# Optimization experiments

Measured on AMD Instinct MI355X. Metric: run time of the kernel, lower is better.

Reference implementation:

```python
import jax, jax.numpy as jnp
import numpy as np

EMBED = 768; HEADS = 12; DH = 64; DEPTH = 6; MLP = 3072
PATCH = (4, 16, 16)
N_PATCH = 2048          # (32/4)*(256/16)*(256/16)
N_REAL = N_PATCH + 1    # + cls token
S_PAD = 4096            # padded to multiple of max segment length
SEGS = [128, 256, 512, 1024, 2048]
RATIOS = [1, 2, 4, 8, 16]
NEG = -1e9


def _ln(x, w, b, eps=1e-5):
    m = jnp.mean(x, -1, keepdims=True)
    v = jnp.mean((x - m) ** 2, -1, keepdims=True)
    return (x - m) / jnp.sqrt(v + eps) * w + b


def dilated_attn(x, wq, bq, wk, bk, wv, bv, wo, bo):
    """LongNet dilated attention: per (segment w, ratio r) branch, split the
    sequence into segments of length w, keep every r-th token with a per-head
    offset (h % r), run dense attention inside the sparse segment, then combine
    branches per position/head with softmax-denominator (lse) weights."""
    B, S, E = x.shape
    q = (x @ wq + bq).reshape(B, S, HEADS, DH)
    k = (x @ wk + bk).reshape(B, S, HEADS, DH)
    v = (x @ wv + bv).reshape(B, S, HEADS, DH)
    scale = 1.0 / np.sqrt(DH).astype(np.float32)
    harr = jnp.arange(HEADS)[:, None]
    outs, lses = [], []
    for w, r in zip(SEGS, RATIOS):
        ns, m = S // w, w // r
        idx = (jnp.arange(HEADS)[:, None] % r) + r * jnp.arange(m)[None, :]  # [H, m]

        def seg(t):
            t = t.reshape(B, ns, w, HEADS, DH).transpose(0, 1, 3, 2, 4)  # B,ns,H,w,D
            return jnp.take_along_axis(t, idx[None, None, :, :, None], axis=3)

        qs, ks, vs = seg(q), seg(k), seg(v)  # [B, ns, H, m, D]
        pos = (jnp.arange(ns) * w)[:, None, None] + idx[None]  # [ns, H, m]
        kmask = jnp.where(pos < N_REAL, 0.0, NEG)  # mask padded keys
        sc = jnp.einsum('bnhqd,bnhkd->bnhqk', qs, ks) * scale + kmask[None, :, :, None, :]
        lse = jax.nn.logsumexp(sc, axis=-1)  # [B, ns, H, m]
        o = jnp.einsum('bnhqk,bnhkd->bnhqd', jax.nn.softmax(sc, axis=-1), vs)
        of = jnp.zeros((B, ns, HEADS, w, DH), x.dtype).at[:, :, harr, idx, :].set(o)
        lf = jnp.full((B, ns, HEADS, w), NEG, x.dtype).at[:, :, harr, idx].set(lse)
        outs.append(of.transpose(0, 1, 3, 2, 4).reshape(B, S, HEADS, DH))
        lses.append(lf.transpose(0, 1, 3, 2).reshape(B, S, HEADS))
    O = jnp.stack(outs)   # [Br, B, S, H, D]
    L = jnp.stack(lses)   # [Br, B, S, H]
    wts = jnp.exp(L - jnp.max(L, 0))
    wts = wts / jnp.sum(wts, 0)
    out = jnp.sum(O * wts[..., None], 0).reshape(B, S, E)
    return out @ wo + bo


def setup_inputs() -> dict:
    key = jax.random.key(0)
    ks = jax.random.split(key, 16)
    f = lambda k, shape: (0.02 * jax.random.normal(k, shape)).astype(jnp.float32)
    z = lambda *s: jnp.zeros(s, jnp.float32)
    o = lambda *s: jnp.ones(s, jnp.float32)
    return {
        'x': jax.random.normal(ks[0], (1, 1, 32, 256, 256), dtype=jnp.float32),
        'conv_w': f(ks[1], (EMBED, 1) + PATCH),
        'conv_b': z(EMBED),
        'cls_token': f(ks[2], (1, 1, EMBED)),
        'pos_embed': f(ks[3], (1, N_REAL, EMBED)),
        'ln1_w': o(DEPTH, EMBED), 'ln1_b': z(DEPTH, EMBED),
        'wq': f(ks[4], (DEPTH, EMBED, EMBED)), 'bq': z(DEPTH, EMBED),
        'wk': f(ks[5], (DEPTH, EMBED, EMBED)), 'bk': z(DEPTH, EMBED),
        'wv': f(ks[6], (DEPTH, EMBED, EMBED)), 'bv': z(DEPTH, EMBED),
        'wo': f(ks[7], (DEPTH, EMBED, EMBED)), 'bo': z(DEPTH, EMBED),
        'ln2_w': o(DEPTH, EMBED), 'ln2_b': z(DEPTH, EMBED),
        'w1': f(ks[8], (DEPTH, EMBED, MLP)), 'b1': z(DEPTH, MLP),
        'w2': f(ks[9], (DEPTH, MLP, EMBED)), 'b2': z(DEPTH, EMBED),
        'lnf_w': o(EMBED), 'lnf_b': z(EMBED),
    }


def reference(x, conv_w, conv_b, cls_token, pos_embed, ln1_w, ln1_b,
              wq, bq, wk, bk, wv, bv, wo, bo, ln2_w, ln2_b,
              w1, b1, w2, b2, lnf_w, lnf_b):
    # 3D patch embed: Conv3d stride=kernel=patch, then flatten spatial -> tokens
    p = jax.lax.conv_general_dilated(
        x, conv_w, window_strides=PATCH, padding='VALID',
        dimension_numbers=('NCDHW', 'OIDHW', 'NCDHW'))
    p = p + conv_b[None, :, None, None, None]
    B = p.shape[0]
    tok = p.reshape(B, EMBED, -1).transpose(0, 2, 1)  # [B, N_PATCH, E]
    tok = tok + pos_embed[:, 1:, :]
    cls = cls_token + pos_embed[:, :1, :]
    h = jnp.concatenate([jnp.broadcast_to(cls, (B, 1, EMBED)), tok], axis=1)
    h = jnp.pad(h, ((0, 0), (0, S_PAD - N_REAL), (0, 0)))  # pad to segment multiple

    params = {'ln1_w': ln1_w, 'ln1_b': ln1_b, 'wq': wq, 'bq': bq, 'wk': wk,
              'bk': bk, 'wv': wv, 'bv': bv, 'wo': wo, 'bo': bo,
              'ln2_w': ln2_w, 'ln2_b': ln2_b, 'w1': w1, 'b1': b1,
              'w2': w2, 'b2': b2}

    def layer(h, pr):
        a = dilated_attn(_ln(h, pr['ln1_w'], pr['ln1_b']),
                         pr['wq'], pr['bq'], pr['wk'], pr['bk'],
                         pr['wv'], pr['bv'], pr['wo'], pr['bo'])
        h = h + a
        f = _ln(h, pr['ln2_w'], pr['ln2_b'])
        f = jax.nn.gelu(f @ pr['w1'] + pr['b1'], approximate=False) @ pr['w2'] + pr['b2']
        return h + f, None

    h, _ = jax.lax.scan(layer, h, params)
    return _ln(h[:, 0], lnf_w, lnf_b)  # [B, EMBED]
```

## Files before the change

kernel.cpp:

```cpp
#include <hip/hip_runtime.h>
#include <math.h>

#define EMBED 768
#define HEADS 12
#define DH 64
#define DEPTH 6
#define MLP_DIM 3072
#define N_REAL 2049
#define SP 2112
#define SPAD 2176
#define NEGV (-1e9f)

typedef __attribute__((ext_vector_type(8))) short short8;
typedef __attribute__((ext_vector_type(4))) float f32x4;
typedef float lds_row_t[33];

__device__ __forceinline__ unsigned short f2bf(float f) {
    union { float f; unsigned u; } x; x.f = f;
    unsigned r = x.u + 0x7FFF + ((x.u >> 16) & 1);
    return (unsigned short)(r >> 16);
}
__device__ __forceinline__ float bf2f(unsigned short s) {
    union { unsigned u; float f; } x; x.u = (unsigned)s << 16;
    return x.f;
}

__device__ __forceinline__ float fast_gelu(float v) {
    const float ax = fabsf(v) * 0.70710678118654752f;
    const float tt = 1.0f / (1.0f + 0.3275911f * ax);
    const float poly = tt * (0.254829592f + tt * (-0.284496736f + tt * (1.421413741f
                       + tt * (-1.453152027f + tt * 1.061405429f))));
    float er = 1.0f - poly * __expf(-ax * ax);
    er = (v < 0.0f) ? -er : er;
    return 0.5f * v * (1.0f + er);
}

__device__ __forceinline__ size_t pidx(int mj, int k, int nkt) {
    return (((size_t)(mj >> 4) * nkt + (k >> 5)) << 9) + (size_t)((((k >> 3) & 3) * 16 + (mj & 15)) * 8 + (k & 7));
}

__device__ __forceinline__ void im2col_body(const float* __restrict__ x,
                                            unsigned short* __restrict__ p, int pi) {
    const int d = pi >> 8, rr = (pi >> 4) & 15, cc = pi & 15;
    const int t = threadIdx.x;
    #pragma unroll
    for (int u = 0; u < 4; ++u) {
        int i = u * 256 + t;
        int kd = i >> 8, kr = (i >> 4) & 15, kc = i & 15;
        float v = x[(size_t)(d * 4 + kd) * 65536 + (rr * 16 + kr) * 256 + (cc * 16 + kc)];
        p[pidx(pi, i, 32)] = f2bf(v);
    }
}

__global__ void im2col_kernel(const float* __restrict__ x, unsigned short* __restrict__ p) {
    im2col_body(x, p, blockIdx.x);
}

__device__ __forceinline__ void pack_KN_body(lds_row_t* lf, const float* __restrict__ src,
                                             unsigned short* __restrict__ dst,
                                             int N, int K, int bn, int bk) {
    const int t = threadIdx.x;
    {
        const int kk = t >> 3, ch = t & 7;
        const float4* s = (const float4*)(src + (size_t)(bk * 32 + kk) * N + bn * 128 + ch * 16);
        float4 v0 = s[0], v1 = s[1], v2 = s[2], v3 = s[3];
        float tmp[16];
        ((float4*)tmp)[0] = v0; ((float4*)tmp)[1] = v1; ((float4*)tmp)[2] = v2; ((float4*)tmp)[3] = v3;
        const int cidx = (kk + 4 * ch) & 31;
        #pragma unroll
        for (int u = 0; u < 16; ++u) lf[ch * 16 + u][cidx] = tmp[u];
    }
    __syncthreads();
    const int nkt = K >> 5;
    const int cg = t >> 5;
    const int lbase = t & 31;
    const int rot = 4 * cg;
    unsigned short* o = dst + (((size_t)(bn * 8 + cg) * nkt + bk) << 9);
    #pragma unroll
    for (int q = 0; q < 2; ++q) {
        const int l = lbase + 32 * q;
        const int col = cg * 16 + (l & 15), kb = (l >> 4) * 8;
        unsigned short ov[8];
        #pragma unroll
        for (int e = 0; e < 8; ++e) ov[e] = f2bf(lf[col][(kb + e + rot) & 31]);
        *(short8*)(o + l * 8) = *(short8*)ov;
    }
    __syncthreads();
}

__device__ __forceinline__ void pack_piece(lds_row_t* lf, int r,
                                           const float* wq, const float* wk,
                                           const float* wv, const float* wo,
                                           const float* w1s, const float* w2s,
                                           unsigned short* qkv_pk, unsigned short* o_pk,
                                           unsigned short* w1_pk, unsigned short* w2_pk) {
    if (r < 576) {
        const int m = r / 144, rr = r % 144;
        const float* src = (m == 0) ? wq : (m == 1) ? wk : (m == 2) ? wv : wo;
        unsigned short* dst = (m < 3) ? qkv_pk + (size_t)m * EMBED * EMBED : o_pk;
        pack_KN_body(lf, src, dst, EMBED, EMBED, rr % 6, rr / 6);
    } else if (r < 1152) {
        const int rr = r - 576;
        pack_KN_body(lf, w1s, w1_pk, MLP_DIM, EMBED, rr % 24, rr / 24);
    } else {
        const int rr = r - 1152;
        pack_KN_body(lf, w2s, w2_pk, EMBED, MLP_DIM, rr % 6, rr / 6);
    }
}

__global__ void pack_all_kernel(const float* __restrict__ wq, const float* __restrict__ wk,
                                const float* __restrict__ wv, const float* __restrict__ wo,
                                const float* __restrict__ w1s, const float* __restrict__ w2s,
                                unsigned short* __restrict__ qkv_pk, unsigned short* __restrict__ o_pk,
                                unsigned short* __restrict__ w1_pk, unsigned short* __restrict__ w2_pk) {
    __shared__ float lf[128][33];
    pack_piece(lf, blockIdx.x, wq, wk, wv, wo, w1s, w2s, qkv_pk, o_pk, w1_pk, w2_pk);
}

__device__ __forceinline__ void pack_NK_body(lds_row_t* lf, const float* __restrict__ src,
                                             unsigned short* __restrict__ dst,
                                             int N, int K, int bn, int bk) {
    const int t = threadIdx.x;
    {
        const int row = t >> 1, hf = t & 1;
        const float4* s = (const float4*)(src + (size_t)(bn * 128 + row) * K + bk * 32 + hf * 16);
        float4 v0 = s[0], v1 = s[1], v2 = s[2], v3 = s[3];
        float tmp[16];
        ((float4*)tmp)[0] = v0; ((float4*)tmp)[1] = v1; ((float4*)tmp)[2] = v2; ((float4*)tmp)[3] = v3;
        #pragma unroll
        for (int u = 0; u < 16; ++u) lf[row][hf * 16 + u] = tmp[u];
    }
    __syncthreads();
    const int nkt = K >> 5;
    const int cg = t >> 5;
    const int lbase = t & 31;
    unsigned short* o = dst + (((size_t)(bn * 8 + cg) * nkt + bk) << 9);
    #pragma unroll
    for (int q = 0; q < 2; ++q) {
        const int l = lbase + 32 * q;
        const int col = cg * 16 + (l & 15), kb = (l >> 4) * 8;
        unsigned short ov[8];
        #pragma unroll
        for (int e = 0; e < 8; ++e) ov[e] = f2bf(lf[col][kb + e]);
        *(short8*)(o + l * 8) = *(short8*)ov;
    }
    __syncthreads();
}

__global__ void pack_NK_kernel(const float* __restrict__ src, unsigned short* __restrict__ dst,
                               int N, int K) {
    __shared__ float lf[128][33];
    pack_NK_body(lf, src, dst, N, K, blockIdx.x, blockIdx.y);
}

__device__ __forceinline__ void init_misc_body(int i,
                                 const float* __restrict__ bq, const float* __restrict__ bk,
                                 const float* __restrict__ bv, float* __restrict__ bqkv,
                                 const float* __restrict__ cls, const float* __restrict__ pos,
                                 float* __restrict__ h, float* __restrict__ tmp) {
    if (i < DEPTH * 2304) {
        int L = i / 2304, j = i - L * 2304;
        float v = (j < 768) ? bq[L * 768 + j] : (j < 1536) ? bk[L * 768 + j - 768] : bv[L * 768 + j - 1536];
        bqkv[i] = v;
    }
    int j = i - DEPTH * 2304;
    if (j >= 0 && j < EMBED) h[j] = cls[j] + pos[j];
    int k2 = j - EMBED;
    if (k2 >= 0 && k2 < 4 * EMBED)
        tmp[(size_t)(k2 / EMBED) * SP * EMBED + (k2 % EMBED)] = 0.0f;
}

__global__ void init_misc_kernel(const float* __restrict__ bq, const float* __restrict__ bk,
                                 const float* __restrict__ bv, float* __restrict__ bqkv,
                                 const float* __restrict__ cls, const float* __restrict__ pos,
                                 float* __restrict__ h, float* __restrict__ tmp) {
    init_misc_body(blockIdx.x * 256 + threadIdx.x, bq, bk, bv, bqkv, cls, pos, h, tmp);
}

__device__ __forceinline__ void pos_copy_body(const float* __restrict__ pos,
                                              float* __restrict__ h, int r) {
    const size_t base = (size_t)(r + 1) * EMBED;
    const int t = threadIdx.x;
    h[base + t]       = pos[base + t];
    h[base + t + 256] = pos[base + t + 256];
    h[base + t + 512] = pos[base + t + 512];
}

__global__ void pos_copy_kernel(const float* __restrict__ pos, float* __restrict__ h) {
    pos_copy_body(pos, h, blockIdx.x);
}

__global__ void prep_mega_kernel(const float* __restrict__ x, const float* __restrict__ conv_w,
                                 const float* __restrict__ wq, const float* __restrict__ wk,
                                 const float* __restrict__ wv, const float* __restrict__ wo,
                                 const float* __restrict__ w1s, const float* __restrict__ w2s,
                                 const float* __restrict__ bq, const float* __restrict__ bk,
                                 const float* __restrict__ bv, const float* __restrict__ cls,
                                 const float* __restrict__ pos,
                                 unsigned short* __restrict__ patch_pk,
                                 unsigned short* __restrict__ convw_pk,
                                 float* __restrict__ bqkv, float* __restrict__ h,
                                 float* __restrict__ tmp,
                                 unsigned short* __restrict__ qkv_pk, unsigned short* __restrict__ o_pk,
                                 unsigned short* __restrict__ w1_pk, unsigned short* __restrict__ w2_pk) {
    __shared__ float lf[128][33];
    const int fid = blockIdx.x;
    const size_t EE = (size_t)EMBED * EMBED, EM = (size_t)EMBED * MLP_DIM;
    if (fid < 6 * 1728) {
        const int lid = fid / 1728, r = fid % 1728;
        pack_piece(lf, r, wq + lid * EE, wk + lid * EE, wv + lid * EE, wo + lid * EE,
                   w1s + lid * EM, w2s + lid * EM,
                   qkv_pk + (size_t)lid * 3 * EE, o_pk + lid * EE,
                   w1_pk + lid * EM, w2_pk + lid * EM);
    } else if (fid < 6 * 1728 + 192) {
        const int r = fid - 6 * 1728;
        pack_NK_body(lf, conv_w, convw_pk, EMBED, 1024, r % 6, r / 6);
    } else if (fid < 6 * 1728 + 192 + 2048) {
        im2col_body(x, patch_pk, fid - (6 * 1728 + 192));
    } else if (fid < 6 * 1728 + 192 + 2048 + 69) {
        const int r = fid - (6 * 1728 + 192 + 2048);
        init_misc_body(r * 256 + threadIdx.x, bq, bk, bv, bqkv, cls, pos, h, tmp);
    } else {
        pos_copy_body(pos, h, fid - (6 * 1728 + 192 + 2048 + 69));
    }
}

template<bool PACKED>
__global__ void ln_res_kernel(float* __restrict__ h, const float* __restrict__ tmp, int nt,
                              void* __restrict__ outv,
                              const float* __restrict__ w, const float* __restrict__ b,
                              int M) {
    int row = blockIdx.x;
    if (row >= M) return;
    const size_t base = (size_t)row * EMBED;
    int tid = threadIdx.x;
    float v0 = h[base + tid], v1 = h[base + tid + 256], v2 = h[base + tid + 512];
    for (int c = 0; c < nt; ++c) {
        const float* tc = tmp + (size_t)c * SP * EMBED + base;
        v0 += tc[tid]; v1 += tc[tid + 256]; v2 += tc[tid + 512];
    }
    h[base + tid] = v0; h[base + tid + 256] = v1; h[base + tid + 512] = v2;
    __shared__ float red[4];
    float s = v0 + v1 + v2;
    #pragma unroll
    for (int o = 32; o > 0; o >>= 1) s += __shfl_down(s, o);
    if ((tid & 63) == 0) red[tid >> 6] = s;
    __syncthreads();
    float mean = (red[0] + red[1] + red[2] + red[3]) * (1.0f / 768.0f);
    __syncthreads();
    float d0 = v0 - mean, d1 = v1 - mean, d2 = v2 - mean;
    float q2 = d0 * d0 + d1 * d1 + d2 * d2;
    #pragma unroll
    for (int o = 32; o > 0; o >>= 1) q2 += __shfl_down(q2, o);
    if ((tid & 63) == 0) red[tid >> 6] = q2;
    __syncthreads();
    float var = (red[0] + red[1] + red[2] + red[3]) * (1.0f / 768.0f);
    float rstd = 1.0f / sqrtf(var + 1e-5f);
    float o0 = d0 * rstd * w[tid]       + b[tid];
    float o1 = d1 * rstd * w[tid + 256] + b[tid + 256];
    float o2 = d2 * rstd * w[tid + 512] + b[tid + 512];
    if (PACKED) {
        unsigned short* o = (unsigned short*)outv;
        o[pidx(row, tid,       24)] = f2bf(o0);
        o[pidx(row, tid + 256, 24)] = f2bf(o1);
        o[pidx(row, tid + 512, 24)] = f2bf(o2);
    } else {
        float* orow = (float*)outv + (size_t)row * EMBED;
        orow[tid] = o0; orow[tid + 256] = o1; orow[tid + 512] = o2;
    }
}

template<int ACT, int MODE>
__global__ __launch_bounds__(256)
void gemm_bf16(const unsigned short* __restrict__ Apk, const unsigned short* __restrict__ Bpk,
               const float* __restrict__ bias, void* __restrict__ Cv,
               int M, int N, int K, int nx, int ny, int nz) {
    const int nwg = nx * ny * nz;
    const int fid = blockIdx.x;
    const int xcd = fid & 7, slot = fid >> 3;
    const int qq = nwg >> 3, rr2 = nwg & 7;
    const int orig = (xcd < rr2 ? xcd * (qq + 1) : rr2 * (qq + 1) + (xcd - rr2) * qq) + slot;
    const int bx = orig % nx;
    const int tzy = orig / nx;
    const int bz = tzy % nz;
    const int by = tzy / nz;

    const int tid = threadIdx.x;
    const int lane = tid & 63;
    const int w4 = tid >> 6;
    const int wm = w4 >> 1, wn = w4 & 1;
    const int row0 = by * 128 + wm * 64, col0 = bx * 128 + wn * 64;
    const int nktT = K >> 5;
    const int nk = nktT / nz;
    const int t0 = bz * nk;

    f32x4 acc[4][4];
    #pragma unroll
    for (int mi = 0; mi < 4; ++mi)
        #pragma unroll
        for (int ni = 0; ni < 4; ++ni)
            #pragma unroll
            for (int j = 0; j < 4; ++j) acc[mi][ni][j] = 0.0f;

    const unsigned short* Ab[4];
    const unsigned short* Bb[4];
    #pragma unroll
    for (int i = 0; i < 4; ++i) {
        Ab[i] = Apk + (((size_t)(by * 8 + wm * 4 + i) * nktT + t0) << 9) + lane * 8;
        Bb[i] = Bpk + (((size_t)(bx * 8 + wn * 4 + i) * nktT + t0) << 9) + lane * 8;
    }

    auto LOADT = [&](int t, short8* aa, short8* bb) {
        #pragma unroll
        for (int i = 0; i < 4; ++i) {
            aa[i] = *(const short8*)(Ab[i] + (size_t)t * 512);
            bb[i] = *(const short8*)(Bb[i] + (size_t)t * 512);
        }
    };
    auto MF = [&](short8* aa, short8* bb) {
        #pragma unroll
        for (int mi = 0; mi < 4; ++mi)
            #pragma unroll
            for (int ni = 0; ni < 4; ++ni)
                acc[mi][ni] = __builtin_amdgcn_mfma_f32_16x16x32_bf16(aa[mi], bb[ni], acc[mi][ni], 0, 0, 0);
    };

    short8 A0[4], B0[4], A1[4], B1[4];
    LOADT(0, A0, B0);
    for (int t = 0; t < nk; t += 2) {
        LOADT(t + 1, A1, B1);
        MF(A0, B0);
        if (t + 2 < nk) LOADT(t + 2, A0, B0);
        MF(A1, B1);
    }

    float* Cf = (float*)Cv + (MODE == 0 ? (size_t)bz * SP * EMBED : 0);
    unsigned short* Cb = (unsigned short*)Cv;
    const int ln15 = lane & 15, kq = lane >> 4;
    const int nktN = N >> 5;
    const bool addb = (bz == 0);
    #pragma unroll
    for (int mi = 0; mi < 4; ++mi) {
        #pragma unroll
        for (int ni = 0; ni < 4; ++ni) {
            const int col = col0 + ni * 16 + ln15;
            const float bb = addb ? bias[col] : 0.0f;
            #pragma unroll
            for (int j = 0; j < 4; ++j) {
                const int row = row0 + mi * 16 + kq * 4 + j;
                if (row < M) {
                    float v = acc[mi][ni][j] + bb;
                    if (ACT == 1) v = fast_gelu(v);
                    if (MODE == 0)      Cf[(size_t)row * N + col] = v;
                    else if (MODE == 2) Cb[(size_t)row * N + col] = f2bf(v);
                    else                Cb[pidx(row, col, nktN)] = f2bf(v);
                }
            }
        }
    }
}

__global__ __launch_bounds__(256, 1)
void attn_kernel(const unsigned short* __restrict__ qkv,
                 unsigned short* __restrict__ Obr, float* __restrict__ Lbr) {
    const int bx = blockIdx.x, hh = blockIdx.y;
    int b, n;
    if      (bx < 17) { b = 0; n = bx; }
    else if (bx < 26) { b = 1; n = bx - 17; }
    else if (bx < 31) { b = 2; n = bx - 26; }
    else if (bx < 34) { b = 3; n = bx - 31; }
    else              { b = 4; n = bx - 34; }
    const int r = 1 << b;
    const int segw = 128 << b;
    const int base = n * segw + (hh & (r - 1));

    __shared__ __attribute__((aligned(16))) unsigned short VT[64 * 128];
    __shared__ __attribute__((aligned(16))) unsigned short Pl[128 * 128];

    const int tid = threadIdx.x;

    {
        const int key = tid >> 1, dh2 = (tid & 1) * 32;
        const int pos = base + r * key;
        const bool val = pos < N_REAL;
        const unsigned short* vsrc = qkv + (size_t)(val ? pos : 0) * 2304 + 1536 + hh * 64 + dh2;
        #pragma unroll
        for (int u = 0; u < 4; ++u) {
            short8 vv = ((const short8*)vsrc)[u];
            #pragma unroll
            for (int e = 0; e < 8; ++e) {
                const int d = dh2 + u * 8 + e;
                VT[(d * 256 + ((key * 2) ^ ((d & 7) << 4))) >> 1] =
                    val ? (unsigned short)vv[e] : (unsigned short)0;
            }
        }
    }
    __syncthreads();

    const int lane = tid & 63, wv = tid >> 6;
    const int ln15 = lane & 15, kq = lane >> 4;

    f32x4 sc[2][8];
    #pragma unroll
    for (int mi = 0; mi < 2; ++mi)
        #pragma unroll
        for (int ni = 0; ni < 8; ++ni)
            #pragma unroll
            for (int j = 0; j < 4; ++j) sc[mi][ni][j] = 0.0f;

    #pragma unroll
    for (int kt = 0; kt < 2; ++kt) {
        short8 qfr[2], kfr[8];
        #pragma unroll
        for (int mi = 0; mi < 2; ++mi) {
            const int pos = base + r * (wv * 32 + mi * 16 + ln15);
            qfr[mi] = *(const short8*)(qkv + (size_t)(pos < N_REAL ? pos : 0) * 2304
                                       + hh * 64 + kt * 32 + kq * 8);
        }
        #pragma unroll
        for (int ni = 0; ni < 8; ++ni) {
            const int pos = base + r * (ni * 16 + ln15);
            kfr[ni] = *(const short8*)(qkv + (size_t)(pos < N_REAL ? pos : 0) * 2304
                                       + 768 + hh * 64 + kt * 32 + kq * 8);
        }
        #pragma unroll
        for (int mi = 0; mi < 2; ++mi)
            #pragma unroll
            for (int ni = 0; ni < 8; ++ni)
                sc[mi][ni] = __builtin_amdgcn_mfma_f32_16x16x32_bf16(qfr[mi], kfr[ni], sc[mi][ni], 0, 0, 0);
    }

    #pragma unroll
    for (int ni = 0; ni < 8; ++ni) {
        const bool kval = (base + r * (ni * 16 + ln15)) < N_REAL;
        #pragma unroll
        for (int mi = 0; mi < 2; ++mi)
            #pragma unroll
            for (int j = 0; j < 4; ++j)
                sc[mi][ni][j] = kval ? sc[mi][ni][j] * 0.125f : NEGV;
    }

    float rsum[2][4];
    #pragma unroll
    for (int mi = 0; mi < 2; ++mi) {
        #pragma unroll
        for (int j = 0; j < 4; ++j) {
            float mx = sc[mi][0][j];
            #pragma unroll
            for (int ni = 1; ni < 8; ++ni) mx = fmaxf(mx, sc[mi][ni][j]);
            mx = fmaxf(mx, __shfl_xor(mx, 1));
            mx = fmaxf(mx, __shfl_xor(mx, 2));
            mx = fmaxf(mx, __shfl_xor(mx, 4));
            mx = fmaxf(mx, __shfl_xor(mx, 8));
            float sm = 0.f;
            #pragma unroll
            for (int ni = 0; ni < 8; ++ni) {
                float e = __expf(sc[mi][ni][j] - mx);
                sc[mi][ni][j] = e;
                sm += e;
            }
            sm += __shfl_xor(sm, 1);
            sm += __shfl_xor(sm, 2);
            sm += __shfl_xor(sm, 4);
            sm += __shfl_xor(sm, 8);
            rsum[mi][j] = sm;
            const int prow = wv * 32 + mi * 16 + kq * 4 + j;
            const int qpos = base + r * prow;
            if (ln15 == 0 && qpos < N_REAL)
                Lbr[((size_t)b * SP + qpos) * HEADS + hh] = mx + logf(sm);
        }
    }

    #pragma unroll
    for (int mi = 0; mi < 2; ++mi)
        #pragma unroll
        for (int j = 0; j < 4; ++j) {
            const int prow = wv * 32 + mi * 16 + kq * 4 + j;
            #pragma unroll
            for (int ni = 0; ni < 8; ++ni) {
                const int col = ni * 16 + ln15;
                Pl[(prow * 256 + ((col * 2) ^ ((prow & 7) << 4))) >> 1] = f2bf(sc[mi][ni][j]);
            }
        }
    __syncthreads();

    f32x4 ov[2][4];
    #pragma unroll
    for (int mi = 0; mi < 2; ++mi)
        #pragma unroll
        for (int ni = 0; ni < 4; ++ni)
            #pragma unroll
            for (int j = 0; j < 4; ++j) ov[mi][ni][j] = 0.0f;

    #pragma unroll
    for (int kt = 0; kt < 4; ++kt) {
        short8 pa[2], vb[4];
        #pragma unroll
        for (int mi = 0; mi < 2; ++mi) {
            const int row = wv * 32 + mi * 16 + ln15;
            pa[mi] = *(const short8*)((const char*)Pl + row * 256
                                      + ((kt * 64 + kq * 16) ^ ((row & 7) << 4)));
        }
        #pragma unroll
        for (int ni = 0; ni < 4; ++ni) {
            const int d = ni * 16 + ln15;
            vb[ni] = *(const short8*)((const char*)VT + d * 256
                                      + ((kt * 64 + kq * 16) ^ ((d & 7) << 4)));
        }
        #pragma unroll
        for (int mi = 0; mi < 2; ++mi)
            #pragma unroll
            for (int ni = 0; ni < 4; ++ni)
                ov[mi][ni] = __builtin_amdgcn_mfma_f32_16x16x32_bf16(pa[mi], vb[ni], ov[mi][ni], 0, 0, 0);
    }

    #pragma unroll
    for (int mi = 0; mi < 2; ++mi)
        #pragma unroll
        for (int j = 0; j < 4; ++j) {
            const int prow = wv * 32 + mi * 16 + kq * 4 + j;
            const int qpos = base + r * prow;
            if (qpos < N_REAL) {
                const float inv = 1.0f / rsum[mi][j];
                #pragma unroll
                for (int ni = 0; ni < 4; ++ni)
                    Obr[((size_t)b * N_REAL + qpos) * EMBED + hh * 64 + ni * 16 + ln15] =
                        f2bf(ov[mi][ni][j] * inv);
            }
        }
}

__global__ void combine_kernel(const unsigned short* __restrict__ Obr, const float* __restrict__ Lbr,
                               unsigned short* __restrict__ out) {
    int gid = blockIdx.x * 256 + threadIdx.x;
    if (gid >= N_REAL * EMBED) return;
    int p = gid / EMBED, e = gid - p * EMBED;
    int h = e >> 6;
    float l[5];
    float mx = NEGV;
    #pragma unroll
    for (int b = 0; b < 5; ++b) {
        const int rm = (1 << b) - 1;
        l[b] = ((p & rm) == (h & rm)) ? Lbr[((size_t)b * SP + p) * HEADS + h] : NEGV;
        mx = fmaxf(mx, l[b]);
    }
    float wsum = 0.f, acc = 0.f;
    #pragma unroll
    for (int b = 0; b < 5; ++b) {
        if (l[b] > NEGV * 0.5f) {
            float wt = expf(l[b] - mx);
            wsum += wt;
            acc += wt * bf2f(Obr[((size_t)b * N_REAL + p) * EMBED + e]);
        }
    }
    out[pidx(p, e, 24)] = f2bf(acc / wsum);
}

extern "C" void kernel_launch(void* const* d_in, const int* in_sizes, int n_in,
                              void* d_out, int out_size, void* d_ws, size_t ws_size,
                              hipStream_t stream) {
    const float* x      = (const float*)d_in[0];
    const float* conv_w = (const float*)d_in[1];
    const float* conv_b = (const float*)d_in[2];
    const float* cls    = (const float*)d_in[3];
    const float* pos    = (const float*)d_in[4];
    const float* ln1w   = (const float*)d_in[5];
    const float* ln1b   = (const float*)d_in[6];
    const float* wq     = (const float*)d_in[7];
    const float* bq     = (const float*)d_in[8];
    const float* wk     = (const float*)d_in[9];
    const float* bk     = (const float*)d_in[10];
    const float* wv     = (const float*)d_in[11];
    const float* bv     = (const float*)d_in[12];
    const float* wo     = (const float*)d_in[13];
    const float* bo     = (const float*)d_in[14];
    const float* ln2w   = (const float*)d_in[15];
    const float* ln2b   = (const float*)d_in[16];
    const float* w1     = (const float*)d_in[17];
    const float* b1     = (const float*)d_in[18];
    const float* w2     = (const float*)d_in[19];
    const float* b2     = (const float*)d_in[20];
    const float* lnfw   = (const float*)d_in[21];
    const float* lnfb   = (const float*)d_in[22];

    const size_t EE = (size_t)EMBED * EMBED;
    const size_t EM = (size_t)EMBED * MLP_DIM;

    const size_t base_floats =
        (size_t)SP * EMBED + 4 * (size_t)SP * EMBED + 5 * (size_t)SP * HEADS
        + (size_t)DEPTH * 2304 + (size_t)SPAD * 2304 / 2 + (size_t)SPAD * EMBED / 2
        + (size_t)SPAD * EMBED / 2 + (size_t)SPAD * MLP_DIM / 2 + (size_t)2112 * 1024 / 2
        + (size_t)EMBED * 1024 / 2 + ((size_t)5 * N_REAL * EMBED / 2 + 64);
    const size_t per_layer_floats = (3 * EE + EE + EM + EM) / 2;
    const bool up = ws_size >= (base_floats + 6 * per_layer_floats) * 4 + (1 << 20);
    const int NL = up ? DEPTH : 1;

    float* ws = (float*)d_ws;
    float* h     = ws;  ws += (size_t)SP * EMBED;
    float* tmp   = ws;  ws += (size_t)4 * SP * EMBED;
    float* Lbr   = ws;  ws += (size_t)5 * SP * HEADS;
    float* bqkv  = ws;  ws += (size_t)DEPTH * 2304;
    unsigned short* qkv_bf   = (unsigned short*)ws;  ws += (size_t)SPAD * 2304 / 2;
    unsigned short* xln_pk   = (unsigned short*)ws;  ws += (size_t)SPAD * EMBED / 2;
    unsigned short* attn_pk  = (unsigned short*)ws;  ws += (size_t)SPAD * EMBED / 2;
    unsigned short* mid_pk   = (unsigned short*)ws;  ws += (size_t)SPAD * MLP_DIM / 2;
    unsigned short* patch_pk = (unsigned short*)ws;  ws += (size_t)2112 * 1024 / 2;
    unsigned short* convw_pk = (unsigned short*)ws;  ws += (size_t)EMBED * 1024 / 2;
    unsigned short* Obr      = (unsigned short*)ws;  ws += (size_t)5 * N_REAL * EMBED / 2 + 64;
    unsigned short* wqkv_pk  = (unsigned short*)ws;  ws += (size_t)NL * 3 * EE / 2;
    unsigned short* wo_pk    = (unsigned short*)ws;  ws += (size_t)NL * EE / 2;
    unsigned short* w1_pk    = (unsigned short*)ws;  ws += (size_t)NL * EM / 2;
    unsigned short* w2_pk    = (unsigned short*)ws;  ws += (size_t)NL * EM / 2;

    if (up) {
        prep_mega_kernel<<<6 * 1728 + 192 + 2048 + 69 + 2048, 256, 0, stream>>>(
            x, conv_w, wq, wk, wv, wo, w1, w2, bq, bk, bv, cls, pos,
            patch_pk, convw_pk, bqkv, h, tmp, wqkv_pk, wo_pk, w1_pk, w2_pk);
    } else {
        im2col_kernel<<<2048, 256, 0, stream>>>(x, patch_pk);
        pack_NK_kernel<<<dim3(6, 32), 256, 0, stream>>>(conv_w, convw_pk, EMBED, 1024);
        init_misc_kernel<<<69, 256, 0, stream>>>(bq, bk, bv, bqkv, cls, pos, h, tmp);
        pos_copy_kernel<<<2048, 256, 0, stream>>>(pos, h);
    }
    gemm_bf16<0, 0><<<384, 256, 0, stream>>>(patch_pk, convw_pk, conv_b,
                                             tmp + EMBED, 2048, EMBED, 1024, 6, 16, 4);

    for (int L = 0; L < DEPTH; ++L) {
        const int off = up ? L : 0;
        unsigned short* qkvW = wqkv_pk + (size_t)off * 3 * EE;
        unsigned short* woW  = wo_pk   + (size_t)off * EE;
        unsigned short* w1W  = w1_pk   + (size_t)off * EM;
        unsigned short* w2W  = w2_pk   + (size_t)off * EM;
        if (!up)
            pack_all_kernel<<<1728, 256, 0, stream>>>(wq + L * EE, wk + L * EE, wv + L * EE,
                                                      wo + L * EE, w1 + L * EM, w2 + L * EM,
                                                      qkvW, woW, w1W, w2W);

        ln_res_kernel<true><<<N_REAL, 256, 0, stream>>>(h, tmp, 4, xln_pk,
                                                        ln1w + (size_t)L * EMBED,
                                                        ln1b + (size_t)L * EMBED, N_REAL);
        gemm_bf16<0, 2><<<306, 256, 0, stream>>>(xln_pk, qkvW, bqkv + (size_t)L * 2304,
                                                 qkv_bf, N_REAL, 2304, EMBED, 18, 17, 1);
        attn_kernel<<<dim3(36, 12), 256, 0, stream>>>(qkv_bf, Obr, Lbr);
        combine_kernel<<<((N_REAL * EMBED) + 255) / 256, 256, 0, stream>>>(Obr, Lbr, attn_pk);
        gemm_bf16<0, 0><<<408, 256, 0, stream>>>(attn_pk, woW, bo + (size_t)L * EMBED,
                                                 tmp, N_REAL, EMBED, EMBED, 6, 17, 4);
        ln_res_kernel<true><<<N_REAL, 256, 0, stream>>>(h, tmp, 4, xln_pk,
                                                        ln2w + (size_t)L * EMBED,
                                                        ln2b + (size_t)L * EMBED, N_REAL);
        gemm_bf16<1, 3><<<408, 256, 0, stream>>>(xln_pk, w1W, b1 + (size_t)L * MLP_DIM,
                                                 mid_pk, N_REAL, MLP_DIM, EMBED, 24, 17, 1);
        gemm_bf16<0, 0><<<408, 256, 0, stream>>>(mid_pk, w2W, b2 + (size_t)L * EMBED,
                                                 tmp, N_REAL, EMBED, MLP_DIM, 6, 17, 4);
    }

    ln_res_kernel<false><<<1, 256, 0, stream>>>(h, tmp, 4, (float*)d_out, lnfw, lnfb, 1);
}
```

Baseline: 908.2 us.

## Fuse branch combine and im2col into GEMM A-operand loads

Removes the standalone combine kernel and the im2col pass. The out-projection GEMM now builds its A tiles directly from the per-branch attention outputs and LSE weights, and the patch-embedding GEMM reads and converts the raw input video on the fly. This drops two intermediate packed buffers and their global round trips, plus a kernel launch per layer. In exchange, the GEMM inner loop does gathered loads, exponentials and bf16 conversion, and the LSE weights are recomputed for every N-tile and K-split, which may slow the GEMM main loop.

Result: slower. 1.351 ms (+48.7%).

```diff
diff --git a/kernel.cpp b/kernel.cpp
--- a/kernel.cpp
+++ b/kernel.cpp
@@ -37,23 +37,6 @@
 
 __device__ __forceinline__ size_t pidx(int mj, int k, int nkt) {
     return (((size_t)(mj >> 4) * nkt + (k >> 5)) << 9) + (size_t)((((k >> 3) & 3) * 16 + (mj & 15)) * 8 + (k & 7));
-}
-
-__device__ __forceinline__ void im2col_body(const float* __restrict__ x,
-                                            unsigned short* __restrict__ p, int pi) {
-    const int d = pi >> 8, rr = (pi >> 4) & 15, cc = pi & 15;
-    const int t = threadIdx.x;
-    #pragma unroll
-    for (int u = 0; u < 4; ++u) {
-        int i = u * 256 + t;
-        int kd = i >> 8, kr = (i >> 4) & 15, kc = i & 15;
-        float v = x[(size_t)(d * 4 + kd) * 65536 + (rr * 16 + kr) * 256 + (cc * 16 + kc)];
-        p[pidx(pi, i, 32)] = f2bf(v);
-    }
-}
-
-__global__ void im2col_kernel(const float* __restrict__ x, unsigned short* __restrict__ p) {
-    im2col_body(x, p, blockIdx.x);
 }
 
 __device__ __forceinline__ void pack_KN_body(lds_row_t* lf, const float* __restrict__ src,
@@ -190,14 +173,13 @@
     pos_copy_body(pos, h, blockIdx.x);
 }
 
-__global__ void prep_mega_kernel(const float* __restrict__ x, const float* __restrict__ conv_w,
+__global__ void prep_mega_kernel(const float* __restrict__ conv_w,
                                  const float* __restrict__ wq, const float* __restrict__ wk,
                                  const float* __restrict__ wv, const float* __restrict__ wo,
                                  const float* __restrict__ w1s, const float* __restrict__ w2s,
                                  const float* __restrict__ bq, const float* __restrict__ bk,
                                  const float* __restrict__ bv, const float* __restrict__ cls,
                                  const float* __restrict__ pos,
-                                 unsigned short* __restrict__ patch_pk,
                                  unsigned short* __restrict__ convw_pk,
                                  float* __restrict__ bqkv, float* __restrict__ h,
                                  float* __restrict__ tmp,
@@ -215,13 +197,11 @@
     } else if (fid < 6 * 1728 + 192) {
         const int r = fid - 6 * 1728;
         pack_NK_body(lf, conv_w, convw_pk, EMBED, 1024, r % 6, r / 6);
-    } else if (fid < 6 * 1728 + 192 + 2048) {
-        im2col_body(x, patch_pk, fid - (6 * 1728 + 192));
-    } else if (fid < 6 * 1728 + 192 + 2048 + 69) {
-        const int r = fid - (6 * 1728 + 192 + 2048);
+    } else if (fid < 6 * 1728 + 192 + 69) {
+        const int r = fid - (6 * 1728 + 192);
         init_misc_body(r * 256 + threadIdx.x, bq, bk, bv, bqkv, cls, pos, h, tmp);
     } else {
-        pos_copy_body(pos, h, fid - (6 * 1728 + 192 + 2048 + 69));
+        pos_copy_body(pos, h, fid - (6 * 1728 + 192 + 69));
     }
 }
 
@@ -270,11 +250,13 @@
     }
 }
 
-template<int ACT, int MODE>
+template<int ACT, int MODE, int ASRC>
 __global__ __launch_bounds__(256)
 void gemm_bf16(const unsigned short* __restrict__ Apk, const unsigned short* __restrict__ Bpk,
                const float* __restrict__ bias, void* __restrict__ Cv,
-               int M, int N, int K, int nx, int ny, int nz) {
+               int M, int N, int K, int nx, int ny, int nz,
+               const unsigned short* __restrict__ ObrP, const float* __restrict__ LbrP,
+               const float* __restrict__ xP) {
     const int nwg = nx * ny * nz;
     const int fid = blockIdx.x;
     const int xcd = fid & 7, slot = fid >> 3;
@@ -293,6 +275,7 @@
     const int nktT = K >> 5;
     const int nk = nktT / nz;
     const int t0 = bz * nk;
+    const int ln15 = lane & 15, kq = lane >> 4;
 
     f32x4 acc[4][4];
     #pragma unroll
@@ -306,15 +289,66 @@
     const unsigned short* Bb[4];
     #pragma unroll
     for (int i = 0; i < 4; ++i) {
-        Ab[i] = Apk + (((size_t)(by * 8 + wm * 4 + i) * nktT + t0) << 9) + lane * 8;
+        if (ASRC == 0)
+            Ab[i] = Apk + (((size_t)(by * 8 + wm * 4 + i) * nktT + t0) << 9) + lane * 8;
         Bb[i] = Bpk + (((size_t)(bx * 8 + wn * 4 + i) * nktT + t0) << 9) + lane * 8;
     }
 
-    auto LOADT = [&](int t, short8* aa, short8* bb) {
+    auto loadA = [&](int i, int trel, short8& out) {
+        if constexpr (ASRC == 0) {
+            out = *(const short8*)(Ab[i] + (size_t)trel * 512);
+        } else if constexpr (ASRC == 1) {
+            const int row = (by * 8 + wm * 4 + i) * 16 + ln15;
+            const int pos = (row < N_REAL) ? row : 0;
+            const int k = (t0 + trel) * 32 + kq * 8;
+            const int hh = k >> 6;
+            float lv[5];
+            float mx = NEGV;
+            #pragma unroll
+            for (int b5 = 0; b5 < 5; ++b5) {
+                const int rm = (1 << b5) - 1;
+                const bool valid = ((pos & rm) == (hh & rm));
+                lv[b5] = valid ? LbrP[((size_t)b5 * SP + pos) * HEADS + hh] : NEGV;
+                mx = fmaxf(mx, lv[b5]);
+            }
+            float wsum = 0.f;
+            float osum[8];
+            #pragma unroll
+            for (int e = 0; e < 8; ++e) osum[e] = 0.f;
+            #pragma unroll
+            for (int b5 = 0; b5 < 5; ++b5) {
+                if (lv[b5] > NEGV * 0.5f) {
+                    const float wgt = __expf(lv[b5] - mx);
+                    wsum += wgt;
+                    short8 v = *(const short8*)(ObrP + ((size_t)b5 * N_REAL + pos) * EMBED + k);
+                    #pragma unroll
+                    for (int e = 0; e < 8; ++e) osum[e] += wgt * bf2f((unsigned short)v[e]);
+                }
+            }
+            const float inv = 1.0f / wsum;
+            unsigned short tv[8];
+            #pragma unroll
+            for (int e = 0; e < 8; ++e) tv[e] = f2bf(osum[e] * inv);
+            out = *(short8*)tv;
+        } else {
+            const int row = (by * 8 + wm * 4 + i) * 16 + ln15;
+            const int k = (t0 + trel) * 32 + kq * 8;
+            const int kd = k >> 8, kr = (k >> 4) & 15, kc = k & 15;
+            const int d = row >> 8, rr = (row >> 4) & 15, cc = row & 15;
+            const float* s = xP + (size_t)(d * 4 + kd) * 65536 + (rr * 16 + kr) * 256 + cc * 16 + kc;
+            float4 aL = ((const float4*)s)[0], aH = ((const float4*)s)[1];
+            unsigned short tv[8];
+            tv[0] = f2bf(aL.x); tv[1] = f2bf(aL.y); tv[2] = f2bf(aL.z); tv[3] = f2bf(aL.w);
+            tv[4] = f2bf(aH.x); tv[5] = f2bf(aH.y); tv[6] = f2bf(aH.z); tv[7] = f2bf(aH.w);
+            out = *(short8*)tv;
+        }
+    };
+
+    auto LOADT = [&](int trel, short8* aa, short8* bb) {
         #pragma unroll
         for (int i = 0; i < 4; ++i) {
-            aa[i] = *(const short8*)(Ab[i] + (size_t)t * 512);
-            bb[i] = *(const short8*)(Bb[i] + (size_t)t * 512);
+            loadA(i, trel, aa[i]);
+            bb[i] = *(const short8*)(Bb[i] + (size_t)trel * 512);
         }
     };
     auto MF = [&](short8* aa, short8* bb) {
@@ -336,7 +370,6 @@
 
     float* Cf = (float*)Cv + (MODE == 0 ? (size_t)bz * SP * EMBED : 0);
     unsigned short* Cb = (unsigned short*)Cv;
-    const int ln15 = lane & 15, kq = lane >> 4;
     const int nktN = N >> 5;
     const bool addb = (bz == 0);
     #pragma unroll
@@ -528,32 +561,6 @@
                         f2bf(ov[mi][ni][j] * inv);
             }
         }
-}
-
-__global__ void combine_kernel(const unsigned short* __restrict__ Obr, const float* __restrict__ Lbr,
-                               unsigned short* __restrict__ out) {
-    int gid = blockIdx.x * 256 + threadIdx.x;
-    if (gid >= N_REAL * EMBED) return;
-    int p = gid / EMBED, e = gid - p * EMBED;
-    int h = e >> 6;
-    float l[5];
-    float mx = NEGV;
-    #pragma unroll
-    for (int b = 0; b < 5; ++b) {
-        const int rm = (1 << b) - 1;
-        l[b] = ((p & rm) == (h & rm)) ? Lbr[((size_t)b * SP + p) * HEADS + h] : NEGV;
-        mx = fmaxf(mx, l[b]);
-    }
-    float wsum = 0.f, acc = 0.f;
-    #pragma unroll
-    for (int b = 0; b < 5; ++b) {
-        if (l[b] > NEGV * 0.5f) {
-            float wt = expf(l[b] - mx);
-            wsum += wt;
-            acc += wt * bf2f(Obr[((size_t)b * N_REAL + p) * EMBED + e]);
-        }
-    }
-    out[pidx(p, e, 24)] = f2bf(acc / wsum);
 }
 
 extern "C" void kernel_launch(void* const* d_in, const int* in_sizes, int n_in,
@@ -589,7 +596,7 @@
     const size_t base_floats =
         (size_t)SP * EMBED + 4 * (size_t)SP * EMBED + 5 * (size_t)SP * HEADS
         + (size_t)DEPTH * 2304 + (size_t)SPAD * 2304 / 2 + (size_t)SPAD * EMBED / 2
-        + (size_t)SPAD * EMBED / 2 + (size_t)SPAD * MLP_DIM / 2 + (size_t)2112 * 1024 / 2
+        + (size_t)SPAD * MLP_DIM / 2
         + (size_t)EMBED * 1024 / 2 + ((size_t)5 * N_REAL * EMBED / 2 + 64);
     const size_t per_layer_floats = (3 * EE + EE + EM + EM) / 2;
     const bool up = ws_size >= (base_floats + 6 * per_layer_floats) * 4 + (1 << 20);
@@ -602,9 +609,7 @@
     float* bqkv  = ws;  ws += (size_t)DEPTH * 2304;
     unsigned short* qkv_bf   = (unsigned short*)ws;  ws += (size_t)SPAD * 2304 / 2;
     unsigned short* xln_pk   = (unsigned short*)ws;  ws += (size_t)SPAD * EMBED / 2;
-    unsigned short* attn_pk  = (unsigned short*)ws;  ws += (size_t)SPAD * EMBED / 2;
     unsigned short* mid_pk   = (unsigned short*)ws;  ws += (size_t)SPAD * MLP_DIM / 2;
-    unsigned short* patch_pk = (unsigned short*)ws;  ws += (size_t)2112 * 1024 / 2;
     unsigned short* convw_pk = (unsigned short*)ws;  ws += (size_t)EMBED * 1024 / 2;
     unsigned short* Obr      = (unsigned short*)ws;  ws += (size_t)5 * N_REAL * EMBED / 2 + 64;
     unsigned short* wqkv_pk  = (unsigned short*)ws;  ws += (size_t)NL * 3 * EE / 2;
@@ -613,17 +618,17 @@
     unsigned short* w2_pk    = (unsigned short*)ws;  ws += (size_t)NL * EM / 2;
 
     if (up) {
-        prep_mega_kernel<<<6 * 1728 + 192 + 2048 + 69 + 2048, 256, 0, stream>>>(
-            x, conv_w, wq, wk, wv, wo, w1, w2, bq, bk, bv, cls, pos,
-            patch_pk, convw_pk, bqkv, h, tmp, wqkv_pk, wo_pk, w1_pk, w2_pk);
+        prep_mega_kernel<<<6 * 1728 + 192 + 69 + 2048, 256, 0, stream>>>(
+            conv_w, wq, wk, wv, wo, w1, w2, bq, bk, bv, cls, pos,
+            convw_pk, bqkv, h, tmp, wqkv_pk, wo_pk, w1_pk, w2_pk);
     } else {
-        im2col_kernel<<<2048, 256, 0, stream>>>(x, patch_pk);
         pack_NK_kernel<<<dim3(6, 32), 256, 0, stream>>>(conv_w, convw_pk, EMBED, 1024);
         init_misc_kernel<<<69, 256, 0, stream>>>(bq, bk, bv, bqkv, cls, pos, h, tmp);
         pos_copy_kernel<<<2048, 256, 0, stream>>>(pos, h);
     }
-    gemm_bf16<0, 0><<<384, 256, 0, stream>>>(patch_pk, convw_pk, conv_b,
-                                             tmp + EMBED, 2048, EMBED, 1024, 6, 16, 4);
+    gemm_bf16<0, 0, 2><<<384, 256, 0, stream>>>(nullptr, convw_pk, conv_b,
+                                                tmp + EMBED, 2048, EMBED, 1024, 6, 16, 4,
+                                                nullptr, nullptr, x);
 
     for (int L = 0; L < DEPTH; ++L) {
         const int off = up ? L : 0;
@@ -639,19 +644,22 @@
         ln_res_kernel<true><<<N_REAL, 256, 0, stream>>>(h, tmp, 4, xln_pk,
                                                         ln1w + (size_t)L * EMBED,
                                                         ln1b + (size_t)L * EMBED, N_REAL);
-        gemm_bf16<0, 2><<<306, 256, 0, stream>>>(xln_pk, qkvW, bqkv + (size_t)L * 2304,
-                                                 qkv_bf, N_REAL, 2304, EMBED, 18, 17, 1);
+        gemm_bf16<0, 2, 0><<<306, 256, 0, stream>>>(xln_pk, qkvW, bqkv + (size_t)L * 2304,
+                                                    qkv_bf, N_REAL, 2304, EMBED, 18, 17, 1,
+                                                    nullptr, nullptr, nullptr);
         attn_kernel<<<dim3(36, 12), 256, 0, stream>>>(qkv_bf, Obr, Lbr);
-        combine_kernel<<<((N_REAL * EMBED) + 255) / 256, 256, 0, stream>>>(Obr, Lbr, attn_pk);
-        gemm_bf16<0, 0><<<408, 256, 0, stream>>>(attn_pk, woW, bo + (size_t)L * EMBED,
-                                                 tmp, N_REAL, EMBED, EMBED, 6, 17, 4);
+        gemm_bf16<0, 0, 1><<<408, 256, 0, stream>>>(nullptr, woW, bo + (size_t)L * EMBED,
+                                                    tmp, N_REAL, EMBED, EMBED, 6, 17, 4,
+                                                    Obr, Lbr, nullptr);
         ln_res_kernel<true><<<N_REAL, 256, 0, stream>>>(h, tmp, 4, xln_pk,
                                                         ln2w + (size_t)L * EMBED,
                                                         ln2b + (size_t)L * EMBED, N_REAL);
-        gemm_bf16<1, 3><<<408, 256, 0, stream>>>(xln_pk, w1W, b1 + (size_t)L * MLP_DIM,
-                                                 mid_pk, N_REAL, MLP_DIM, EMBED, 24, 17, 1);
-        gemm_bf16<0, 0><<<408, 256, 0, stream>>>(mid_pk, w2W, b2 + (size_t)L * EMBED,
-                                                 tmp, N_REAL, EMBED, MLP_DIM, 6, 17, 4);
+        gemm_bf16<1, 3, 0><<<408, 256, 0, stream>>>(xln_pk, w1W, b1 + (size_t)L * MLP_DIM,
+                                                    mid_pk, N_REAL, MLP_DIM, EMBED, 24, 17, 1,
+                                                    nullptr, nullptr, nullptr);
+        gemm_bf16<0, 0, 0><<<408, 256, 0, stream>>>(mid_pk, w2W, b2 + (size_t)L * EMBED,
+                                                    tmp, N_REAL, EMBED, MLP_DIM, 6, 17, 4,
+                                                    nullptr, nullptr, nullptr);
     }
 
     ln_res_kernel<false><<<1, 256, 0, stream>>>(h, tmp, 4, (float*)d_out, lnfw, lnfb, 1);
```
